# Kernel optimization log

Hardware: AMD Instinct MI355X
Metric: run time of the kernel (lower is better)

## Reference

```python
import jax, jax.numpy as jnp
import numpy as np

N = 1024      # nodes
IN = 64       # input_dim
H = 128       # hidden_dim
L = 4         # num graph layers
HEADS = 4     # MHA heads


def setup_inputs() -> dict:
    key = jax.random.key(0)
    ks = jax.random.split(key, 12)
    s = lambda k, shape: (jax.random.normal(k, shape, dtype=jnp.float32) * 0.05)
    z = lambda shape: jnp.zeros(shape, jnp.float32)
    return {
        "x": jax.random.normal(ks[0], (N, IN), dtype=jnp.float32),
        "emb_W": s(ks[1], (IN, H)), "emb_b": z((H,)),
        "ln_g": jnp.ones((H,), jnp.float32), "ln_b": z((H,)),
        "edge_W1": s(ks[2], (2 * H, H)), "edge_b1": z((H,)),
        "edge_W2": s(ks[3], (H, 1)), "edge_b2": z((1,)),
        "gc_W": s(ks[4], (L, H, H)), "gc_b": z((L, H)),
        "in_proj_W": s(ks[5], (3 * H, H)), "in_proj_b": z((3 * H,)),
        "out_proj_W": s(ks[6], (H, H)), "out_proj_b": z((H,)),
        "out_W": s(ks[7], (H, 6)), "out_b": z((6,)),
    }


def reference(x, emb_W, emb_b, ln_g, ln_b, edge_W1, edge_b1, edge_W2, edge_b2,
              gc_W, gc_b, in_proj_W, in_proj_b, out_proj_W, out_proj_b,
              out_W, out_b):
    # node embedding: Linear -> LayerNorm -> ReLU
    h = x @ emb_W + emb_b
    mu = h.mean(-1, keepdims=True)
    var = ((h - mu) ** 2).mean(-1, keepdims=True)
    h = (h - mu) * jax.lax.rsqrt(var + 1e-5) * ln_g + ln_b
    h = jax.nn.relu(h)

    n, Hd = h.shape
    # dynamic graph: edge MLP on concat(x_i, x_j) for all pairs, batched.
    # cat([x_i, x_j]) @ W1 == x_i @ W1[:H] + x_j @ W1[H:]
    a = h @ edge_W1[:Hd]          # [n, H]
    b = h @ edge_W1[Hd:]          # [n, H]
    e = jax.nn.relu(a[:, None, :] + b[None, :, :] + edge_b1)   # [n, n, H]
    adj = jax.nn.sigmoid(jnp.einsum('ijh,ho->ijo', e, edge_W2)[..., 0] + edge_b2[0])
    adj = adj * (1.0 - jnp.eye(n, dtype=adj.dtype))             # no self-edges

    # physics-informed graph conv layers: adj @ (h @ W) + b
    for l in range(gc_W.shape[0]):
        h = adj @ (h @ gc_W[l]) + gc_b[l]

    # MultiheadAttention (self-attention, seq=n, batch=1)
    d = Hd // HEADS
    qkv = h @ in_proj_W.T + in_proj_b
    q, k, v = jnp.split(qkv, 3, axis=-1)
    q = q.reshape(n, HEADS, d).transpose(1, 0, 2)   # [h, n, d]
    k = k.reshape(n, HEADS, d).transpose(1, 0, 2)
    v = v.reshape(n, HEADS, d).transpose(1, 0, 2)
    scale = 1.0 / np.sqrt(d).astype(np.float32)
    attn = jax.nn.softmax(jnp.einsum('hnd,hmd->hnm', q, k) * scale, axis=-1)
    o = jnp.einsum('hnm,hmd->hnd', attn, v).transpose(1, 0, 2).reshape(n, Hd)
    h = o @ out_proj_W.T + out_proj_b

    # pooled head + per-metric activations
    out = h.mean(0) @ out_W + out_b                 # [6]
    sig = jax.nn.sigmoid(out)
    return jnp.stack([sig[0], jax.nn.relu(out[1]), sig[2], sig[3], sig[4], sig[5]])
```

## Files before the change

kernel.cpp:

```cpp
#include <hip/hip_runtime.h>
#include <math.h>

#define NN 1024
#define IN_DIM 64
#define H 128
#define NL 4
#define HEADS 4
#define DH 32

__global__ void k_transpose(const float* __restrict__ inW, const float* __restrict__ outW,
                            float* __restrict__ Wt_in, float* __restrict__ Wt_out) {
    int idx = blockIdx.x * blockDim.x + threadIdx.x;
    if (idx < 384 * 128) {
        int k = idx / 384, m = idx % 384;
        Wt_in[idx] = inW[m * 128 + k];
    }
    int idx2 = idx - 384 * 128;
    if (idx2 >= 0 && idx2 < 128 * 128) {
        int k = idx2 / 128, c = idx2 % 128;
        Wt_out[idx2] = outW[c * 128 + k];
    }
}

__global__ __launch_bounds__(128) void k_embed(const float* __restrict__ x,
        const float* __restrict__ embW, const float* __restrict__ embB,
        const float* __restrict__ lng, const float* __restrict__ lnb,
        const float* __restrict__ eW1, const float* __restrict__ eb1,
        const float* __restrict__ gcW0,
        float* __restrict__ aM, float* __restrict__ bM, float* __restrict__ g0) {
    __shared__ float xs[IN_DIM];
    __shared__ float hs[H];
    __shared__ float red[H];
    int i = blockIdx.x, t = threadIdx.x;
    if (t < IN_DIM) xs[t] = x[i * IN_DIM + t];
    __syncthreads();
    float acc = embB[t];
    #pragma unroll 8
    for (int k = 0; k < IN_DIM; ++k) acc = fmaf(xs[k], embW[k * H + t], acc);
    red[t] = acc; __syncthreads();
    for (int s = 64; s > 0; s >>= 1) { if (t < s) red[t] += red[t + s]; __syncthreads(); }
    float mu = red[0] * (1.f / H);
    __syncthreads();
    float d = acc - mu;
    red[t] = d * d; __syncthreads();
    for (int s = 64; s > 0; s >>= 1) { if (t < s) red[t] += red[t + s]; __syncthreads(); }
    float var = red[0] * (1.f / H);
    float hv = d * rsqrtf(var + 1e-5f) * lng[t] + lnb[t];
    hv = fmaxf(hv, 0.f);
    hs[t] = hv;
    __syncthreads();
    float aa = eb1[t], bb = 0.f, gg = 0.f;
    #pragma unroll 8
    for (int k = 0; k < H; ++k) {
        float hk = hs[k];
        aa = fmaf(hk, eW1[k * H + t], aa);
        bb = fmaf(hk, eW1[(H + k) * H + t], bb);
        gg = fmaf(hk, gcW0[k * H + t], gg);
    }
    aM[i * H + t] = aa;
    bM[i * H + t] = bb;
    g0[i * H + t] = gg;
}

#define AT 32
__global__ __launch_bounds__(256) void k_adj(const float* __restrict__ aM, const float* __restrict__ bM,
        const float* __restrict__ w2, const float* __restrict__ eb2p, float* __restrict__ adj) {
    __shared__ float as_[AT][H + 4];
    __shared__ float bst[H][AT + 4];
    __shared__ float w2s[H];
    int i0 = blockIdx.y * AT, j0 = blockIdx.x * AT;
    int t = threadIdx.x;
    for (int idx = t; idx < AT * H; idx += 256) {
        int r = idx >> 7, c = idx & 127;
        as_[r][c] = aM[(i0 + r) * H + c];
        bst[c][r] = bM[(j0 + r) * H + c];
    }
    if (t < H) w2s[t] = w2[t];
    __syncthreads();
    int ti = t >> 3, tjg = t & 7;
    float a0 = 0.f, a1 = 0.f, a2 = 0.f, a3 = 0.f;
    const float eb2 = eb2p[0];
    #pragma unroll 4
    for (int h = 0; h < H; ++h) {
        float av = as_[ti][h];
        float4 bv = *(const float4*)&bst[h][tjg * 4];
        float wh = w2s[h];
        a0 = fmaf(fmaxf(av + bv.x, 0.f), wh, a0);
        a1 = fmaf(fmaxf(av + bv.y, 0.f), wh, a1);
        a2 = fmaf(fmaxf(av + bv.z, 0.f), wh, a2);
        a3 = fmaf(fmaxf(av + bv.w, 0.f), wh, a3);
    }
    int i = i0 + ti, jb = j0 + tjg * 4;
    float4 ov;
    ov.x = (i == jb + 0) ? 0.f : 1.f / (1.f + __expf(-(a0 + eb2)));
    ov.y = (i == jb + 1) ? 0.f : 1.f / (1.f + __expf(-(a1 + eb2)));
    ov.z = (i == jb + 2) ? 0.f : 1.f / (1.f + __expf(-(a2 + eb2)));
    ov.w = (i == jb + 3) ? 0.f : 1.f / (1.f + __expf(-(a3 + eb2)));
    *(float4*)&adj[(size_t)i * NN + jb] = ov;
}

__global__ void k_rowmat(const float* __restrict__ inM, const float* __restrict__ W,
        const float* __restrict__ bias, float* __restrict__ outM, int K, int C) {
    extern __shared__ float rs[];
    int i = blockIdx.x, t = threadIdx.x;
    for (int k = t; k < K; k += blockDim.x) rs[k] = inM[i * K + k];
    __syncthreads();
    float acc = bias ? bias[t] : 0.f;
    #pragma unroll 8
    for (int k = 0; k < K; ++k) acc = fmaf(rs[k], W[k * C + t], acc);
    outM[i * C + t] = acc;
}

#define RT 8
#define JC 256
__global__ __launch_bounds__(256) void k_spmm(const float* __restrict__ adj, const float* __restrict__ g,
        float* __restrict__ partial) {
    __shared__ float adjs[RT][JC];
    __shared__ float redbuf[RT][H];
    int rt = blockIdx.x;
    int p = blockIdx.y;
    int t = threadIdx.x;
    int c = t & 127, half = t >> 7;
    int r0 = rt * RT;
    for (int idx = t; idx < RT * JC; idx += 256) {
        int r = idx >> 8, j = idx & 255;
        adjs[r][j] = adj[(size_t)(r0 + r) * NN + p * JC + j];
    }
    __syncthreads();
    int jbase = half * 128;
    int j0 = p * JC + jbase;
    float acc[RT];
    #pragma unroll
    for (int r = 0; r < RT; ++r) acc[r] = 0.f;
    #pragma unroll 8
    for (int jj = 0; jj < 128; ++jj) {
        float gv = g[(j0 + jj) * H + c];
        int ja = jbase + jj;
        #pragma unroll
        for (int r = 0; r < RT; ++r) acc[r] = fmaf(adjs[r][ja], gv, acc[r]);
    }
    if (half == 1) {
        #pragma unroll
        for (int r = 0; r < RT; ++r) redbuf[r][c] = acc[r];
    }
    __syncthreads();
    if (half == 0) {
        #pragma unroll
        for (int r = 0; r < RT; ++r)
            partial[((size_t)p * NN + r0 + r) * H + c] = acc[r] + redbuf[r][c];
    }
}

__global__ __launch_bounds__(128) void k_redmat128(const float* __restrict__ partial,
        const float* __restrict__ bias, const float* __restrict__ W, float* __restrict__ outM) {
    __shared__ float s[H];
    int i = blockIdx.x, t = threadIdx.x;
    float v = partial[i * H + t] + partial[NN * H + i * H + t]
            + partial[2 * NN * H + i * H + t] + partial[3 * NN * H + i * H + t] + bias[t];
    s[t] = v;
    __syncthreads();
    float acc = 0.f;
    #pragma unroll 8
    for (int k = 0; k < H; ++k) acc = fmaf(s[k], W[k * H + t], acc);
    outM[i * H + t] = acc;
}

__global__ __launch_bounds__(384) void k_redmat384(const float* __restrict__ partial,
        const float* __restrict__ bias, const float* __restrict__ W,
        const float* __restrict__ bias2, float* __restrict__ outM) {
    __shared__ float s[H];
    int i = blockIdx.x, t = threadIdx.x;
    if (t < H) {
        float v = partial[i * H + t] + partial[NN * H + i * H + t]
                + partial[2 * NN * H + i * H + t] + partial[3 * NN * H + i * H + t] + bias[t];
        s[t] = v;
    }
    __syncthreads();
    float acc = bias2[t];
    #pragma unroll 8
    for (int k = 0; k < H; ++k) acc = fmaf(s[k], W[k * 384 + t], acc);
    outM[i * 384 + t] = acc;
}

#define QR 8
#define KC 128
#define KSPLIT 8
__global__ __launch_bounds__(256) void k_attn_part(const float* __restrict__ qkv,
        float* __restrict__ opart, float* __restrict__ mpart, float* __restrict__ lpart) {
    __shared__ float qs[QR][DH + 4];
    __shared__ float ks[KC][DH + 1];
    __shared__ float vs[KC][DH + 1];
    __shared__ float ss[QR][KC + 4];
    int head = blockIdx.y;
    int i0 = blockIdx.x * QR;
    int kp = blockIdx.z;
    int j0 = kp * KC;
    int t = threadIdx.x;
    int qoff = head * DH, koff = 128 + head * DH, voff = 256 + head * DH;
    for (int idx = t; idx < KC * DH; idx += 256) {
        int r = idx >> 5, d = idx & 31;
        ks[r][d] = qkv[(j0 + r) * 384 + koff + d];
        vs[r][d] = qkv[(j0 + r) * 384 + voff + d];
    }
    {
        int r = t >> 5, d = t & 31;
        qs[r][d] = qkv[(i0 + r) * 384 + qoff + d];
    }
    __syncthreads();
    const float scale = 0.17677669529663687f;
    {
        int jj = t & 127, rb = (t >> 7) * 4;
        float s0 = 0.f, s1 = 0.f, s2 = 0.f, s3 = 0.f;
        #pragma unroll
        for (int kk = 0; kk < DH; ++kk) {
            float kv = ks[jj][kk];
            s0 = fmaf(qs[rb + 0][kk], kv, s0);
            s1 = fmaf(qs[rb + 1][kk], kv, s1);
            s2 = fmaf(qs[rb + 2][kk], kv, s2);
            s3 = fmaf(qs[rb + 3][kk], kv, s3);
        }
        ss[rb + 0][jj] = s0 * scale;
        ss[rb + 1][jj] = s1 * scale;
        ss[rb + 2][jj] = s2 * scale;
        ss[rb + 3][jj] = s3 * scale;
    }
    __syncthreads();
    int r_ = t >> 5, d_ = t & 31;
    float sv0 = ss[r_][d_], sv1 = ss[r_][d_ + 32], sv2 = ss[r_][d_ + 64], sv3 = ss[r_][d_ + 96];
    float m = fmaxf(fmaxf(sv0, sv1), fmaxf(sv2, sv3));
    #pragma unroll
    for (int off = 16; off > 0; off >>= 1) m = fmaxf(m, __shfl_xor(m, off, 32));
    float p0 = __expf(sv0 - m), p1 = __expf(sv1 - m), p2 = __expf(sv2 - m), p3 = __expf(sv3 - m);
    ss[r_][d_] = p0; ss[r_][d_ + 32] = p1; ss[r_][d_ + 64] = p2; ss[r_][d_ + 96] = p3;
    float l = p0 + p1 + p2 + p3;
    #pragma unroll
    for (int off = 16; off > 0; off >>= 1) l += __shfl_xor(l, off, 32);
    float o0 = 0.f, o1 = 0.f, o2 = 0.f, o3 = 0.f;
    #pragma unroll 4
    for (int j = 0; j < KC; j += 4) {
        o0 = fmaf(ss[r_][j + 0], vs[j + 0][d_], o0);
        o1 = fmaf(ss[r_][j + 1], vs[j + 1][d_], o1);
        o2 = fmaf(ss[r_][j + 2], vs[j + 2][d_], o2);
        o3 = fmaf(ss[r_][j + 3], vs[j + 3][d_], o3);
    }
    float o = (o0 + o1) + (o2 + o3);
    int pidx = head * KSPLIT + kp;
    opart[((size_t)pidx * NN + i0 + r_) * DH + d_] = o;
    if (d_ == 0) {
        mpart[pidx * NN + i0 + r_] = m;
        lpart[pidx * NN + i0 + r_] = l;
    }
}

__global__ void k_attn_merge(const float* __restrict__ opart, const float* __restrict__ mpart,
        const float* __restrict__ lpart, float* __restrict__ attn_o) {
    int gid = blockIdx.x * 256 + threadIdx.x;
    int d = gid & 31;
    int row = (gid >> 5) & 1023;
    int head = gid >> 15;
    float mv[KSPLIT];
    float M = -1e30f;
    #pragma unroll
    for (int p = 0; p < KSPLIT; ++p) {
        mv[p] = mpart[(head * KSPLIT + p) * NN + row];
        M = fmaxf(M, mv[p]);
    }
    float L = 0.f, o = 0.f;
    #pragma unroll
    for (int p = 0; p < KSPLIT; ++p) {
        float w = __expf(mv[p] - M);
        L = fmaf(lpart[(head * KSPLIT + p) * NN + row], w, L);
        o = fmaf(opart[((size_t)(head * KSPLIT + p) * NN + row) * DH + d], w, o);
    }
    attn_o[row * H + head * DH + d] = o / L;
}

__global__ void k_pool1(const float* __restrict__ h2, float* __restrict__ pp) {
    int b = blockIdx.x;
    int t = threadIdx.x;
    int c = t & 127, rg = t >> 7;
    int r0 = b * 32 + rg * 16;
    float s = 0.f;
    #pragma unroll
    for (int r = 0; r < 16; ++r) s += h2[(r0 + r) * H + c];
    pp[(b * 2 + rg) * H + c] = s;
}

__global__ void k_pool2(const float* __restrict__ pp, const float* __restrict__ outW,
        const float* __restrict__ outB, float* __restrict__ out) {
    __shared__ float pooled[H];
    int t = threadIdx.x;
    float s = 0.f;
    #pragma unroll 8
    for (int p = 0; p < 64; ++p) s += pp[p * H + t];
    pooled[t] = s * (1.f / 1024.f);
    __syncthreads();
    if (t < 6) {
        float acc = outB[t];
        for (int c = 0; c < H; ++c) acc = fmaf(pooled[c], outW[c * 6 + t], acc);
        out[t] = (t == 1) ? fmaxf(acc, 0.f) : 1.f / (1.f + expf(-acc));
    }
}

extern "C" void kernel_launch(void* const* d_in, const int* in_sizes, int n_in,
                              void* d_out, int out_size, void* d_ws, size_t ws_size,
                              hipStream_t stream) {
    const float* x       = (const float*)d_in[0];
    const float* emb_W   = (const float*)d_in[1];
    const float* emb_b   = (const float*)d_in[2];
    const float* ln_g    = (const float*)d_in[3];
    const float* ln_b    = (const float*)d_in[4];
    const float* edge_W1 = (const float*)d_in[5];
    const float* edge_b1 = (const float*)d_in[6];
    const float* edge_W2 = (const float*)d_in[7];
    const float* edge_b2 = (const float*)d_in[8];
    const float* gc_W    = (const float*)d_in[9];
    const float* gc_b    = (const float*)d_in[10];
    const float* in_proj_W  = (const float*)d_in[11];
    const float* in_proj_b  = (const float*)d_in[12];
    const float* out_proj_W = (const float*)d_in[13];
    const float* out_proj_b = (const float*)d_in[14];
    const float* out_W   = (const float*)d_in[15];
    const float* out_b   = (const float*)d_in[16];
    float* out = (float*)d_out;

    float* ws = (float*)d_ws;
    float* aM      = ws;
    float* bM      = aM + NN * H;
    float* adj     = bM + NN * H;
    float* g       = adj + NN * NN;
    float* partial = g + NN * H;
    float* qkv     = partial + 4 * NN * H;
    float* Wt_in   = qkv + NN * 384;
    float* Wt_out  = Wt_in + 128 * 384;
    float* pp      = Wt_out + 128 * 128;
    float* opart  = adj;
    float* mpart  = aM;
    float* lpart  = aM + 32 * NN;
    float* attn_o = bM;
    float* h2     = g;

    k_transpose<<<256, 256, 0, stream>>>(in_proj_W, out_proj_W, Wt_in, Wt_out);
    k_embed<<<NN, 128, 0, stream>>>(x, emb_W, emb_b, ln_g, ln_b, edge_W1, edge_b1,
                                    gc_W, aM, bM, g);
    k_adj<<<dim3(NN / AT, NN / AT), 256, 0, stream>>>(aM, bM, edge_W2, edge_b2, adj);

    for (int l = 0; l < NL; ++l) {
        k_spmm<<<dim3(NN / RT, 4), 256, 0, stream>>>(adj, g, partial);
        if (l < NL - 1)
            k_redmat128<<<NN, 128, 0, stream>>>(partial, gc_b + (size_t)l * H,
                                                gc_W + (size_t)(l + 1) * H * H, g);
        else
            k_redmat384<<<NN, 384, 0, stream>>>(partial, gc_b + (size_t)l * H,
                                                Wt_in, in_proj_b, qkv);
    }

    k_attn_part<<<dim3(NN / QR, HEADS, KSPLIT), 256, 0, stream>>>(qkv, opart, mpart, lpart);
    k_attn_merge<<<HEADS * NN * DH / 256, 256, 0, stream>>>(opart, mpart, lpart, attn_o);
    k_rowmat<<<NN, 128, H * sizeof(float), stream>>>(attn_o, Wt_out, out_proj_b, h2, H, 128);
    k_pool1<<<32, 256, 0, stream>>>(h2, pp);
    k_pool2<<<1, 128, 0, stream>>>(pp, out_W, out_b, out);
}
```

Before: 164.1 us.

## Register-tile spmm and attention, fuse transpose into embed and merge with out-proj

```diff
diff --git a/kernel.cpp b/kernel.cpp
--- a/kernel.cpp
+++ b/kernel.cpp
@@ -7,31 +7,28 @@
 #define NL 4
 #define HEADS 4
 #define DH 32
-
-__global__ void k_transpose(const float* __restrict__ inW, const float* __restrict__ outW,
-                            float* __restrict__ Wt_in, float* __restrict__ Wt_out) {
-    int idx = blockIdx.x * blockDim.x + threadIdx.x;
-    if (idx < 384 * 128) {
-        int k = idx / 384, m = idx % 384;
-        Wt_in[idx] = inW[m * 128 + k];
-    }
-    int idx2 = idx - 384 * 128;
-    if (idx2 >= 0 && idx2 < 128 * 128) {
-        int k = idx2 / 128, c = idx2 % 128;
-        Wt_out[idx2] = outW[c * 128 + k];
-    }
-}
+#define KSPLIT 8
+#define NSPLIT 16
 
 __global__ __launch_bounds__(128) void k_embed(const float* __restrict__ x,
         const float* __restrict__ embW, const float* __restrict__ embB,
         const float* __restrict__ lng, const float* __restrict__ lnb,
         const float* __restrict__ eW1, const float* __restrict__ eb1,
         const float* __restrict__ gcW0,
+        const float* __restrict__ inW, const float* __restrict__ outW,
+        float* __restrict__ Wt_in, float* __restrict__ Wt_out,
         float* __restrict__ aM, float* __restrict__ bM, float* __restrict__ g0) {
     __shared__ float xs[IN_DIM];
     __shared__ float hs[H];
     __shared__ float red[H];
     int i = blockIdx.x, t = threadIdx.x;
+    int gidx = i * 128 + t;
+    if (gidx < 49152) {
+        Wt_in[gidx] = inW[(gidx % 384) * 128 + gidx / 384];
+    } else if (gidx < 65536) {
+        int i2 = gidx - 49152;
+        Wt_out[i2] = outW[(i2 % 128) * 128 + i2 / 128];
+    }
     if (t < IN_DIM) xs[t] = x[i * IN_DIM + t];
     __syncthreads();
     float acc = embB[t];
@@ -99,55 +96,39 @@
     *(float4*)&adj[(size_t)i * NN + jb] = ov;
 }
 
-__global__ void k_rowmat(const float* __restrict__ inM, const float* __restrict__ W,
-        const float* __restrict__ bias, float* __restrict__ outM, int K, int C) {
-    extern __shared__ float rs[];
-    int i = blockIdx.x, t = threadIdx.x;
-    for (int k = t; k < K; k += blockDim.x) rs[k] = inM[i * K + k];
-    __syncthreads();
-    float acc = bias ? bias[t] : 0.f;
-    #pragma unroll 8
-    for (int k = 0; k < K; ++k) acc = fmaf(rs[k], W[k * C + t], acc);
-    outM[i * C + t] = acc;
-}
-
-#define RT 8
-#define JC 256
-__global__ __launch_bounds__(256) void k_spmm(const float* __restrict__ adj, const float* __restrict__ g,
+__global__ __launch_bounds__(128) void k_spmm(const float* __restrict__ adj, const float* __restrict__ g,
         float* __restrict__ partial) {
-    __shared__ float adjs[RT][JC];
-    __shared__ float redbuf[RT][H];
-    int rt = blockIdx.x;
-    int p = blockIdx.y;
+    __shared__ float adjs[16][65];
+    int r0 = blockIdx.x * 16;
+    int j0 = blockIdx.y * 64;
     int t = threadIdx.x;
-    int c = t & 127, half = t >> 7;
-    int r0 = rt * RT;
-    for (int idx = t; idx < RT * JC; idx += 256) {
-        int r = idx >> 8, j = idx & 255;
-        adjs[r][j] = adj[(size_t)(r0 + r) * NN + p * JC + j];
-    }
-    __syncthreads();
-    int jbase = half * 128;
-    int j0 = p * JC + jbase;
-    float acc[RT];
-    #pragma unroll
-    for (int r = 0; r < RT; ++r) acc[r] = 0.f;
-    #pragma unroll 8
-    for (int jj = 0; jj < 128; ++jj) {
-        float gv = g[(j0 + jj) * H + c];
-        int ja = jbase + jj;
-        #pragma unroll
-        for (int r = 0; r < RT; ++r) acc[r] = fmaf(adjs[r][ja], gv, acc[r]);
-    }
-    if (half == 1) {
-        #pragma unroll
-        for (int r = 0; r < RT; ++r) redbuf[r][c] = acc[r];
-    }
-    __syncthreads();
-    if (half == 0) {
-        #pragma unroll
-        for (int r = 0; r < RT; ++r)
-            partial[((size_t)p * NN + r0 + r) * H + c] = acc[r] + redbuf[r][c];
+    #pragma unroll
+    for (int it = 0; it < 2; ++it) {
+        int idx = t + it * 128;
+        int r = idx >> 4, jg = idx & 15;
+        float4 av = *(const float4*)&adj[(size_t)(r0 + r) * NN + j0 + jg * 4];
+        adjs[r][jg * 4 + 0] = av.x; adjs[r][jg * 4 + 1] = av.y;
+        adjs[r][jg * 4 + 2] = av.z; adjs[r][jg * 4 + 3] = av.w;
+    }
+    __syncthreads();
+    int rg = t >> 5, cg = t & 31;
+    int c0 = cg * 4;
+    float acc[4][4] = {};
+    #pragma unroll 4
+    for (int jj = 0; jj < 64; ++jj) {
+        float ga[4];
+        *(float4*)ga = *(const float4*)&g[(j0 + jj) * H + c0];
+        #pragma unroll
+        for (int r = 0; r < 4; ++r) {
+            float av = adjs[rg * 4 + r][jj];
+            #pragma unroll
+            for (int c = 0; c < 4; ++c) acc[r][c] = fmaf(av, ga[c], acc[r][c]);
+        }
+    }
+    #pragma unroll
+    for (int r = 0; r < 4; ++r) {
+        float4 ov = {acc[r][0], acc[r][1], acc[r][2], acc[r][3]};
+        *(float4*)&partial[((size_t)blockIdx.y * NN + r0 + rg * 4 + r) * H + c0] = ov;
     }
 }
 
@@ -155,8 +136,9 @@
         const float* __restrict__ bias, const float* __restrict__ W, float* __restrict__ outM) {
     __shared__ float s[H];
     int i = blockIdx.x, t = threadIdx.x;
-    float v = partial[i * H + t] + partial[NN * H + i * H + t]
-            + partial[2 * NN * H + i * H + t] + partial[3 * NN * H + i * H + t] + bias[t];
+    float v = bias[t];
+    #pragma unroll
+    for (int p = 0; p < NSPLIT; ++p) v += partial[(size_t)p * NN * H + i * H + t];
     s[t] = v;
     __syncthreads();
     float acc = 0.f;
@@ -171,8 +153,9 @@
     __shared__ float s[H];
     int i = blockIdx.x, t = threadIdx.x;
     if (t < H) {
-        float v = partial[i * H + t] + partial[NN * H + i * H + t]
-                + partial[2 * NN * H + i * H + t] + partial[3 * NN * H + i * H + t] + bias[t];
+        float v = bias[t];
+        #pragma unroll
+        for (int p = 0; p < NSPLIT; ++p) v += partial[(size_t)p * NN * H + i * H + t];
         s[t] = v;
     }
     __syncthreads();
@@ -182,82 +165,112 @@
     outM[i * 384 + t] = acc;
 }
 
-#define QR 8
-#define KC 128
-#define KSPLIT 8
 __global__ __launch_bounds__(256) void k_attn_part(const float* __restrict__ qkv,
         float* __restrict__ opart, float* __restrict__ mpart, float* __restrict__ lpart) {
-    __shared__ float qs[QR][DH + 4];
-    __shared__ float ks[KC][DH + 1];
-    __shared__ float vs[KC][DH + 1];
-    __shared__ float ss[QR][KC + 4];
-    int head = blockIdx.y;
-    int i0 = blockIdx.x * QR;
-    int kp = blockIdx.z;
-    int j0 = kp * KC;
-    int t = threadIdx.x;
-    int qoff = head * DH, koff = 128 + head * DH, voff = 256 + head * DH;
-    for (int idx = t; idx < KC * DH; idx += 256) {
-        int r = idx >> 5, d = idx & 31;
-        ks[r][d] = qkv[(j0 + r) * 384 + koff + d];
-        vs[r][d] = qkv[(j0 + r) * 384 + voff + d];
-    }
-    {
-        int r = t >> 5, d = t & 31;
-        qs[r][d] = qkv[(i0 + r) * 384 + qoff + d];
-    }
-    __syncthreads();
+    __shared__ float kob[4][32][36];
+    __shared__ float qT[32][36];
+    __shared__ float pT[128][36];
+    __shared__ float marr[32], larr[32];
+    float* kT = &kob[0][0][0];
+    const int t = threadIdx.x;
+    const int head = blockIdx.y, kp = blockIdx.z;
+    const int i0 = blockIdx.x * 32, j0 = kp * 128;
+    const int qoff = head * DH, koff = H + head * DH, voff = 2 * H + head * DH;
     const float scale = 0.17677669529663687f;
     {
-        int jj = t & 127, rb = (t >> 7) * 4;
-        float s0 = 0.f, s1 = 0.f, s2 = 0.f, s3 = 0.f;
-        #pragma unroll
-        for (int kk = 0; kk < DH; ++kk) {
-            float kv = ks[jj][kk];
-            s0 = fmaf(qs[rb + 0][kk], kv, s0);
-            s1 = fmaf(qs[rb + 1][kk], kv, s1);
-            s2 = fmaf(qs[rb + 2][kk], kv, s2);
-            s3 = fmaf(qs[rb + 3][kk], kv, s3);
+        int qi = t >> 3, dg = t & 7;
+        float4 qv = *(const float4*)&qkv[(i0 + qi) * 384 + qoff + dg * 4];
+        qT[dg * 4 + 0][qi] = qv.x * scale;
+        qT[dg * 4 + 1][qi] = qv.y * scale;
+        qT[dg * 4 + 2][qi] = qv.z * scale;
+        qT[dg * 4 + 3][qi] = qv.w * scale;
+    }
+    #pragma unroll
+    for (int it = 0; it < 4; ++it) {
+        int idx = t + it * 256;
+        int j = idx >> 3, dg = idx & 7;
+        float4 kv = *(const float4*)&qkv[(j0 + j) * 384 + koff + dg * 4];
+        kT[(dg * 4 + 0) * 132 + j] = kv.x;
+        kT[(dg * 4 + 1) * 132 + j] = kv.y;
+        kT[(dg * 4 + 2) * 132 + j] = kv.z;
+        kT[(dg * 4 + 3) * 132 + j] = kv.w;
+    }
+    __syncthreads();
+    const int tq = t >> 5, tj = t & 31;
+    float s[4][4] = {};
+    #pragma unroll
+    for (int kk = 0; kk < DH; ++kk) {
+        float qa[4], ka[4];
+        *(float4*)qa = *(float4*)&qT[kk][tq * 4];
+        *(float4*)ka = *(float4*)&kT[kk * 132 + tj * 4];
+        #pragma unroll
+        for (int a = 0; a < 4; ++a)
+            #pragma unroll
+            for (int b = 0; b < 4; ++b) s[a][b] = fmaf(qa[a], ka[b], s[a][b]);
+    }
+    #pragma unroll
+    for (int a = 0; a < 4; ++a) {
+        float mm = fmaxf(fmaxf(s[a][0], s[a][1]), fmaxf(s[a][2], s[a][3]));
+        #pragma unroll
+        for (int off = 16; off > 0; off >>= 1) mm = fmaxf(mm, __shfl_xor(mm, off));
+        float ll = 0.f;
+        #pragma unroll
+        for (int b = 0; b < 4; ++b) { s[a][b] = __expf(s[a][b] - mm); ll += s[a][b]; }
+        #pragma unroll
+        for (int off = 16; off > 0; off >>= 1) ll += __shfl_xor(ll, off);
+        if (tj == 0) { marr[tq * 4 + a] = mm; larr[tq * 4 + a] = ll; }
+    }
+    #pragma unroll
+    for (int b = 0; b < 4; ++b)
+        #pragma unroll
+        for (int a = 0; a < 4; ++a) pT[tj * 4 + b][tq * 4 + a] = s[a][b];
+    __syncthreads();
+    const int qg = t >> 5, dg = (t >> 2) & 7, st = t & 3;
+    float o[4][4] = {};
+    #pragma unroll 4
+    for (int jj = 0; jj < 32; ++jj) {
+        int j = st * 32 + jj;
+        float pa[4], va[4];
+        *(float4*)pa = *(float4*)&pT[j][qg * 4];
+        *(float4*)va = *(const float4*)&qkv[(j0 + j) * 384 + voff + dg * 4];
+        #pragma unroll
+        for (int a = 0; a < 4; ++a)
+            #pragma unroll
+            for (int b = 0; b < 4; ++b) o[a][b] = fmaf(pa[a], va[b], o[a][b]);
+    }
+    #pragma unroll
+    for (int a = 0; a < 4; ++a)
+        #pragma unroll
+        for (int b = 0; b < 4; ++b) kob[st][qg * 4 + a][dg * 4 + b] = o[a][b];
+    __syncthreads();
+    {
+        int q = t >> 3, d0 = (t & 7) * 4;
+        float r0[4], r1[4], r2[4], r3[4];
+        *(float4*)r0 = *(float4*)&kob[0][q][d0];
+        *(float4*)r1 = *(float4*)&kob[1][q][d0];
+        *(float4*)r2 = *(float4*)&kob[2][q][d0];
+        *(float4*)r3 = *(float4*)&kob[3][q][d0];
+        float4 ov;
+        ov.x = (r0[0] + r1[0]) + (r2[0] + r3[0]);
+        ov.y = (r0[1] + r1[1]) + (r2[1] + r3[1]);
+        ov.z = (r0[2] + r1[2]) + (r2[2] + r3[2]);
+        ov.w = (r0[3] + r1[3]) + (r2[3] + r3[3]);
+        int pidx = head * KSPLIT + kp;
+        *(float4*)&opart[((size_t)pidx * NN + i0 + q) * DH + d0] = ov;
+        if (t < 32) {
+            mpart[pidx * NN + i0 + t] = marr[t];
+            lpart[pidx * NN + i0 + t] = larr[t];
         }
-        ss[rb + 0][jj] = s0 * scale;
-        ss[rb + 1][jj] = s1 * scale;
-        ss[rb + 2][jj] = s2 * scale;
-        ss[rb + 3][jj] = s3 * scale;
-    }
-    __syncthreads();
-    int r_ = t >> 5, d_ = t & 31;
-    float sv0 = ss[r_][d_], sv1 = ss[r_][d_ + 32], sv2 = ss[r_][d_ + 64], sv3 = ss[r_][d_ + 96];
-    float m = fmaxf(fmaxf(sv0, sv1), fmaxf(sv2, sv3));
-    #pragma unroll
-    for (int off = 16; off > 0; off >>= 1) m = fmaxf(m, __shfl_xor(m, off, 32));
-    float p0 = __expf(sv0 - m), p1 = __expf(sv1 - m), p2 = __expf(sv2 - m), p3 = __expf(sv3 - m);
-    ss[r_][d_] = p0; ss[r_][d_ + 32] = p1; ss[r_][d_ + 64] = p2; ss[r_][d_ + 96] = p3;
-    float l = p0 + p1 + p2 + p3;
-    #pragma unroll
-    for (int off = 16; off > 0; off >>= 1) l += __shfl_xor(l, off, 32);
-    float o0 = 0.f, o1 = 0.f, o2 = 0.f, o3 = 0.f;
-    #pragma unroll 4
-    for (int j = 0; j < KC; j += 4) {
-        o0 = fmaf(ss[r_][j + 0], vs[j + 0][d_], o0);
-        o1 = fmaf(ss[r_][j + 1], vs[j + 1][d_], o1);
-        o2 = fmaf(ss[r_][j + 2], vs[j + 2][d_], o2);
-        o3 = fmaf(ss[r_][j + 3], vs[j + 3][d_], o3);
-    }
-    float o = (o0 + o1) + (o2 + o3);
-    int pidx = head * KSPLIT + kp;
-    opart[((size_t)pidx * NN + i0 + r_) * DH + d_] = o;
-    if (d_ == 0) {
-        mpart[pidx * NN + i0 + r_] = m;
-        lpart[pidx * NN + i0 + r_] = l;
-    }
-}
-
-__global__ void k_attn_merge(const float* __restrict__ opart, const float* __restrict__ mpart,
-        const float* __restrict__ lpart, float* __restrict__ attn_o) {
-    int gid = blockIdx.x * 256 + threadIdx.x;
-    int d = gid & 31;
-    int row = (gid >> 5) & 1023;
-    int head = gid >> 15;
+    }
+}
+
+__global__ __launch_bounds__(128) void k_mergeproj(const float* __restrict__ opart,
+        const float* __restrict__ mpart, const float* __restrict__ lpart,
+        const float* __restrict__ Wt_out, const float* __restrict__ bias,
+        float* __restrict__ h2) {
+    __shared__ float s[H];
+    int row = blockIdx.x, t = threadIdx.x;
+    int head = t >> 5, d = t & 31;
     float mv[KSPLIT];
     float M = -1e30f;
     #pragma unroll
@@ -272,7 +285,12 @@
         L = fmaf(lpart[(head * KSPLIT + p) * NN + row], w, L);
         o = fmaf(opart[((size_t)(head * KSPLIT + p) * NN + row) * DH + d], w, o);
     }
-    attn_o[row * H + head * DH + d] = o / L;
+    s[t] = o / L;
+    __syncthreads();
+    float acc = bias[t];
+    #pragma unroll 8
+    for (int k = 0; k < H; ++k) acc = fmaf(s[k], Wt_out[k * H + t], acc);
+    h2[row * H + t] = acc;
 }
 
 __global__ void k_pool1(const float* __restrict__ h2, float* __restrict__ pp) {
@@ -330,23 +348,22 @@
     float* adj     = bM + NN * H;
     float* g       = adj + NN * NN;
     float* partial = g + NN * H;
-    float* qkv     = partial + 4 * NN * H;
+    float* qkv     = partial + (size_t)NSPLIT * NN * H;
     float* Wt_in   = qkv + NN * 384;
     float* Wt_out  = Wt_in + 128 * 384;
     float* pp      = Wt_out + 128 * 128;
-    float* opart  = adj;
-    float* mpart  = aM;
-    float* lpart  = aM + 32 * NN;
-    float* attn_o = bM;
-    float* h2     = g;
-
-    k_transpose<<<256, 256, 0, stream>>>(in_proj_W, out_proj_W, Wt_in, Wt_out);
+    float* opart = adj;
+    float* mpart = aM;
+    float* lpart = aM + 32 * NN;
+    float* h2    = g;
+
     k_embed<<<NN, 128, 0, stream>>>(x, emb_W, emb_b, ln_g, ln_b, edge_W1, edge_b1,
-                                    gc_W, aM, bM, g);
+                                    gc_W, in_proj_W, out_proj_W, Wt_in, Wt_out,
+                                    aM, bM, g);
     k_adj<<<dim3(NN / AT, NN / AT), 256, 0, stream>>>(aM, bM, edge_W2, edge_b2, adj);
 
     for (int l = 0; l < NL; ++l) {
-        k_spmm<<<dim3(NN / RT, 4), 256, 0, stream>>>(adj, g, partial);
+        k_spmm<<<dim3(NN / 16, NSPLIT), 128, 0, stream>>>(adj, g, partial);
         if (l < NL - 1)
             k_redmat128<<<NN, 128, 0, stream>>>(partial, gc_b + (size_t)l * H,
                                                 gc_W + (size_t)(l + 1) * H * H, g);
@@ -355,9 +372,8 @@
                                                 Wt_in, in_proj_b, qkv);
     }
 
-    k_attn_part<<<dim3(NN / QR, HEADS, KSPLIT), 256, 0, stream>>>(qkv, opart, mpart, lpart);
-    k_attn_merge<<<HEADS * NN * DH / 256, 256, 0, stream>>>(opart, mpart, lpart, attn_o);
-    k_rowmat<<<NN, 128, H * sizeof(float), stream>>>(attn_o, Wt_out, out_proj_b, h2, H, 128);
+    k_attn_part<<<dim3(NN / 32, HEADS, KSPLIT), 256, 0, stream>>>(qkv, opart, mpart, lpart);
+    k_mergeproj<<<NN, 128, 0, stream>>>(opart, mpart, lpart, Wt_out, out_proj_b, h2);
     k_pool1<<<32, 256, 0, stream>>>(h2, pp);
     k_pool2<<<1, 128, 0, stream>>>(pp, out_W, out_b, out);
 }
```

Result: faster. 159.3 us (-3.0%).
